# Optimization experiments

Measured on AMD Instinct MI355X. Metric: run time of the kernel, lower is better.

## Reference

```python
import jax, jax.numpy as jnp
import numpy as np

# ---- constants (match init_kwargs) ----
H = 16            # bit depth of location codes
TP = 8            # number of parallel location dims
N = 1 << H        # location magnitude bound
N_K = 2
N_C = 2 * H * N_K + 1   # 65 candidate locations per token
T = 512           # T_train
N_TTNBR = 64
K_VOCAB = 128
S = N_TTNBR + K_VOCAB   # 192
D = 256           # dim_eu
TEMP = 0.05


def cos_similarity(c1, c2):
    """CritiGraph frexp-based cosine: sign product * (1 - bitlength(|a|^|b| + 1)/h)."""
    sg = (2 * (c1 >= 0).astype(jnp.int32) - 1) * (2 * (c2 >= 0).astype(jnp.int32) - 1)
    x = jnp.abs(c1) ^ jnp.abs(c2)
    _, e = jnp.frexp((x + 1).astype(jnp.float32))  # exponent == bit_length(x+1)
    return sg.astype(jnp.float32) * (1.0 - e.astype(jnp.float32) / H)


def setup_inputs() -> dict:
    key = jax.random.key(0)
    ks = jax.random.split(key, 8)
    loc = lambda k, shape: jax.random.randint(k, shape, 1 - N, N, dtype=jnp.int32)
    return {
        "cur_tar": jax.random.randint(ks[0], (T,), 0, K_VOCAB, dtype=jnp.int32),
        "cnc_loc": loc(ks[1], (T, N_C, TP)),
        "sta_loc": loc(ks[2], (T, TP)),
        "ttn_loc": loc(ks[3], (T, N_TTNBR, TP)),
        "voc_loc": loc(ks[4], (T, K_VOCAB, TP)),
        "sta_emb": 0.1 * jax.random.normal(ks[5], (T, D), dtype=jnp.float32),
        "ttn_emb": 0.1 * jax.random.normal(ks[6], (T, N_TTNBR, D), dtype=jnp.float32),
        "voc_emb": 0.1 * jax.random.normal(ks[7], (T, K_VOCAB, D), dtype=jnp.float32),
    }


def reference(cur_tar, cnc_loc, sta_loc, ttn_loc, voc_loc, sta_emb, ttn_emb, voc_emb):
    # positives = dynamic neighbors ++ sampled vocab
    pos_loc = jnp.concatenate([ttn_loc, voc_loc], axis=1)      # (T, S, TP) int32
    pos_emb = jnp.concatenate([ttn_emb, voc_emb], axis=1)      # (T, S, D)

    # Euclidean-space logits
    eu_val = 20.0 * TEMP * jnp.einsum('td,tsd->ts', sta_emb, pos_emb)  # (T, S)

    # CT-space similarities
    cos_sp = cos_similarity(sta_loc[:, None, :], pos_loc)      # (T, S, TP)
    cos_sum = cos_sp.sum(axis=-1)                              # (T, S)
    # candidate location swapped into each track d (ct_val_triton math)
    cos_cp = cos_similarity(cnc_loc[:, None, :, :], pos_loc[:, :, None, :])  # (T, S, N_C, TP)
    ct_val = (cos_sum[:, :, None, None] - cos_sp[:, :, None, :] + cos_cp) / TP \
             * (20.0 * TEMP)                                   # (T, S, N_C, TP)

    # KL(eu || ct) over the dynamic neighbors
    logits_ct_dyn = ct_val[:, :N_TTNBR]                        # (T, Nn, N_C, TP)
    logits_eu_dyn = eu_val[:, :N_TTNBR]                        # (T, Nn)
    p_eu = jax.nn.softmax(logits_eu_dyn, axis=1)
    lp_eu = jax.nn.log_softmax(logits_eu_dyn, axis=1)
    lp_ct = jax.nn.log_softmax(logits_ct_dyn, axis=1)
    loss_dyn_dyn = (p_eu[:, :, None, None] * (lp_eu[:, :, None, None] - lp_ct)).sum(axis=1)  # (T, N_C, TP)

    # cross-entropy over the sampled vocab
    logits_ct_sta = ct_val[:, N_TTNBR:] / TEMP                 # (T, K, N_C, TP)
    logits_flat = logits_ct_sta.reshape(T, K_VOCAB, N_C * TP)
    log_probs = jax.nn.log_softmax(logits_flat, axis=1)        # (T, K, N_C*TP)
    idx = jnp.broadcast_to(cur_tar[:, None, None].astype(jnp.int32), (T, 1, N_C * TP))
    target_lp = jnp.take_along_axis(log_probs, idx, axis=1)[:, 0, :]  # (T, N_C*TP)
    loss_dyn_sta = -target_lp.reshape(T, N_C, TP)              # (T, N_C, TP)

    return loss_dyn_dyn, loss_dyn_sta
```

## Files before the change

kernel.cpp:

```cpp
#include <hip/hip_runtime.h>


#define Tn   512
#define NC   65
#define TPd  8
#define NTn  64
#define KV   128
#define Sn   192
#define Dn   256

__global__ __launch_bounds__(256) void critigraph_kernel(
    const int*   __restrict__ cur_tar,
    const int*   __restrict__ cnc_loc,
    const int*   __restrict__ sta_loc,
    const int*   __restrict__ ttn_loc,
    const int*   __restrict__ voc_loc,
    const float* __restrict__ sta_emb,
    const float* __restrict__ ttn_emb,
    float*       __restrict__ out)
{
    __shared__ int   s_apos[Sn * TPd];
    __shared__ float s_base[Sn * TPd];
    __shared__ float s_csum[Sn];
    __shared__ float s_peu[NTn];
    __shared__ float s_eu[NTn];
    __shared__ int   s_cnc[NC * TPd];
    __shared__ int   s_sta[TPd];
    __shared__ float s_kl;

    const int t    = blockIdx.x;
    const int tid  = threadIdx.x;
    const int lane = tid & 63;
    const int wv   = tid >> 6;

    if (tid < TPd) {
        int v = sta_loc[t * TPd + tid];
        s_sta[tid] = (v < 0) ? (int)(0x80000000u | (unsigned)(-v)) : v;
    }
    for (int i = tid; i < NC * TPd; i += 256) {
        int v = cnc_loc[t * NC * TPd + i];
        s_cnc[i] = (v < 0) ? (int)(0x80000000u | (unsigned)(-v)) : v;
    }
    __syncthreads();

    for (int i = tid; i < Sn * TPd; i += 256) {
        int s = i >> 3;
        int v = (s < NTn) ? ttn_loc[t * NTn * TPd + i]
                          : voc_loc[t * KV * TPd + (i - NTn * TPd)];
        int packed = (v < 0) ? (int)(0x80000000u | (unsigned)(-v)) : v;
        s_apos[i] = packed;
        int   y    = packed ^ s_sta[i & 7];
        int   x    = (y & 0x7fffffff) + 1;
        float fclz = (float)__clz(x);
        float c    = fmaf(fclz, 0.0625f, -1.0f);
        c = __int_as_float(__float_as_int(c) ^ (y & 0x80000000));
        s_base[i] = c;
    }
    __syncthreads();

    if (tid < Sn) {
        float a = 0.f;
        #pragma unroll
        for (int p = 0; p < TPd; ++p) a += s_base[tid * TPd + p];
        s_csum[tid] = a;
    }
    __syncthreads();

    for (int i = tid; i < Sn * TPd; i += 256) {
        int s = i >> 3;
        float scale = (s < NTn) ? 0.125f : 2.5f;
        s_base[i] = (s_csum[s] - s_base[i]) * scale;
    }

    {
        const float4* a4 = (const float4*)(sta_emb + (size_t)t * Dn);
        float4 a = a4[lane];
        for (int s = wv; s < NTn; s += 4) {
            const float4* b4 = (const float4*)(ttn_emb + ((size_t)t * NTn + s) * Dn);
            float4 b = b4[lane];
            float d = a.x * b.x + a.y * b.y + a.z * b.z + a.w * b.w;
            #pragma unroll
            for (int m = 1; m < 64; m <<= 1) d += __shfl_xor(d, m);
            if (lane == 0) s_eu[s] = d;
        }
    }
    __syncthreads();

    if (tid < 64) {
        float e  = s_eu[tid];
        float mx = e;
        #pragma unroll
        for (int m = 1; m < 64; m <<= 1) mx = fmaxf(mx, __shfl_xor(mx, m));
        float ex = __expf(e - mx);
        float z  = ex;
        #pragma unroll
        for (int m = 1; m < 64; m <<= 1) z += __shfl_xor(z, m);
        float pe = ex / z;
        s_peu[tid] = pe;
        float kls = pe * ((e - mx) - __logf(z));
        #pragma unroll
        for (int m = 1; m < 64; m <<= 1) kls += __shfl_xor(kls, m);
        if (tid == 0) s_kl = kls;
    }
    __syncthreads();

    const int   tar = cur_tar[t];
    const float kl  = s_kl;
    const int   g   = lane >> 3;
    const int   sub = lane & 7;
    float* out_dd = out + (size_t)t * NC * TPd;
    float* out_ds = out + (size_t)Tn * NC * TPd + (size_t)t * NC * TPd;

    for (int r = wv; r < NC; r += 4) {
        const int acnc = s_cnc[r * TPd + g];

        float sum = 0.f, dot = 0.f;
        #pragma unroll
        for (int k = 0; k < 8; ++k) {
            int   s    = sub + 8 * k;
            int   y    = s_apos[s * TPd + g] ^ acnc;
            int   x    = (y & 0x7fffffff) + 1;
            float fclz = (float)__clz(x);
            float cc   = fmaf(fclz, 0.0078125f, -0.125f);
            cc = __int_as_float(__float_as_int(cc) ^ (y & 0x80000000));
            float ct = s_base[s * TPd + g] + cc;
            sum += __expf(ct);
            dot  = fmaf(s_peu[s], ct, dot);
        }
        #pragma unroll
        for (int m = 1; m < 8; m <<= 1) {
            sum += __shfl_xor(sum, m);
            dot += __shfl_xor(dot, m);
        }
        float loss_dd = kl - dot + __logf(sum);

        float sum2 = 0.f, tgt = 0.f;
        #pragma unroll
        for (int k = 0; k < 16; ++k) {
            int   vv   = sub + 8 * k;
            int   s    = NTn + vv;
            int   y    = s_apos[s * TPd + g] ^ acnc;
            int   x    = (y & 0x7fffffff) + 1;
            float fclz = (float)__clz(x);
            float cc   = fmaf(fclz, 0.15625f, -2.5f);
            cc = __int_as_float(__float_as_int(cc) ^ (y & 0x80000000));
            float ct20 = s_base[s * TPd + g] + cc;
            sum2 += __expf(ct20);
            tgt = (vv == tar) ? ct20 : tgt;
        }
        #pragma unroll
        for (int m = 1; m < 8; m <<= 1) {
            sum2 += __shfl_xor(sum2, m);
            tgt  += __shfl_xor(tgt, m);
        }
        if (sub == 0) {
            out_dd[r * TPd + g] = loss_dd;
            out_ds[r * TPd + g] = __logf(sum2) - tgt;
        }
    }
}

extern "C" void kernel_launch(void* const* d_in, const int* in_sizes, int n_in,
                              void* d_out, int out_size, void* d_ws, size_t ws_size,
                              hipStream_t stream) {
    (void)in_sizes; (void)n_in; (void)d_ws; (void)ws_size; (void)out_size;
    const int*   cur_tar = (const int*)  d_in[0];
    const int*   cnc_loc = (const int*)  d_in[1];
    const int*   sta_loc = (const int*)  d_in[2];
    const int*   ttn_loc = (const int*)  d_in[3];
    const int*   voc_loc = (const int*)  d_in[4];
    const float* sta_emb = (const float*)d_in[5];
    const float* ttn_emb = (const float*)d_in[6];
    critigraph_kernel<<<Tn, 256, 0, stream>>>(cur_tar, cnc_loc, sta_loc, ttn_loc,
                                              voc_loc, sta_emb, ttn_emb, (float*)d_out);
}
```

Measured before the change: 155.8 us.

## Split candidate rows across two blocks per token and hoist invariant work to registers

Launches two blocks per token, each handling about half of the 65 candidate rows, which doubles grid parallelism but makes both blocks redo the per-token setup (location packing, base cosines, embedding dot, softmax). Folds log2e into the constants so it can use hardware exp2/log2. Interleaves loc and base into an int2 shared array and caches each lane's positives in registers across rows. Replaces the per-row dot and target selection with a precomputed per-track dot base plus a single target lookup. It also adds a launch-bounds occupancy hint, which raises register pressure because of the register-cached arrays.

Result: no change. 155.9 us (+0.0%).

```diff
diff --git a/kernel.cpp b/kernel.cpp
--- a/kernel.cpp
+++ b/kernel.cpp
@@ -9,7 +9,22 @@
 #define Sn   192
 #define Dn   256
 
-__global__ __launch_bounds__(256) void critigraph_kernel(
+#define LOG2E 1.44269504088896340736f
+#define LN2   0.69314718055994530942f
+#define K1D (0.0625f * 0.125f * LOG2E)
+#define K0D (-0.125f * LOG2E)
+#define K1S (0.0625f * 2.5f * LOG2E)
+#define K0S (-2.5f * LOG2E)
+
+__device__ __forceinline__ float exp2_fast(float x) {
+#if __has_builtin(__builtin_amdgcn_exp2f)
+    return __builtin_amdgcn_exp2f(x);
+#else
+    return exp2f(x);
+#endif
+}
+
+__global__ __launch_bounds__(256, 4) void critigraph_kernel(
     const int*   __restrict__ cur_tar,
     const int*   __restrict__ cnc_loc,
     const int*   __restrict__ sta_loc,
@@ -19,16 +34,21 @@
     const float* __restrict__ ttn_emb,
     float*       __restrict__ out)
 {
-    __shared__ int   s_apos[Sn * TPd];
-    __shared__ float s_base[Sn * TPd];
+    __shared__ int2  s_ab[Sn * TPd];
     __shared__ float s_csum[Sn];
     __shared__ float s_peu[NTn];
     __shared__ float s_eu[NTn];
     __shared__ int   s_cnc[NC * TPd];
     __shared__ int   s_sta[TPd];
+    __shared__ float s_dotbase[TPd];
     __shared__ float s_kl;
 
-    const int t    = blockIdx.x;
+    const int bx   = blockIdx.x;
+    const int t    = bx >> 1;
+    const int half = bx & 1;
+    const int c0   = half ? 33 : 0;
+    const int c1   = half ? NC : 33;
+
     const int tid  = threadIdx.x;
     const int lane = tid & 63;
     const int wv   = tid >> 6;
@@ -48,30 +68,13 @@
         int v = (s < NTn) ? ttn_loc[t * NTn * TPd + i]
                           : voc_loc[t * KV * TPd + (i - NTn * TPd)];
         int packed = (v < 0) ? (int)(0x80000000u | (unsigned)(-v)) : v;
-        s_apos[i] = packed;
         int   y    = packed ^ s_sta[i & 7];
         int   x    = (y & 0x7fffffff) + 1;
         float fclz = (float)__clz(x);
         float c    = fmaf(fclz, 0.0625f, -1.0f);
         c = __int_as_float(__float_as_int(c) ^ (y & 0x80000000));
-        s_base[i] = c;
-    }
-    __syncthreads();
-
-    if (tid < Sn) {
-        float a = 0.f;
-        #pragma unroll
-        for (int p = 0; p < TPd; ++p) a += s_base[tid * TPd + p];
-        s_csum[tid] = a;
-    }
-    __syncthreads();
-
-    for (int i = tid; i < Sn * TPd; i += 256) {
-        int s = i >> 3;
-        float scale = (s < NTn) ? 0.125f : 2.5f;
-        s_base[i] = (s_csum[s] - s_base[i]) * scale;
-    }
-
+        s_ab[i] = make_int2(packed, __float_as_int(c));
+    }
     {
         const float4* a4 = (const float4*)(sta_emb + (size_t)t * Dn);
         float4 a = a4[lane];
@@ -86,6 +89,20 @@
     }
     __syncthreads();
 
+    if (tid < Sn) {
+        float a = 0.f;
+        #pragma unroll
+        for (int p = 0; p < TPd; ++p) a += __int_as_float(s_ab[tid * TPd + p].y);
+        s_csum[tid] = a;
+    }
+    __syncthreads();
+
+    for (int i = tid; i < Sn * TPd; i += 256) {
+        int s = i >> 3;
+        float sc = (s < NTn) ? (0.125f * LOG2E) : (2.5f * LOG2E);
+        float sp = __int_as_float(s_ab[i].y);
+        s_ab[i].y = __float_as_int((s_csum[s] - sp) * sc);
+    }
     if (tid < 64) {
         float e  = s_eu[tid];
         float mx = e;
@@ -104,58 +121,85 @@
     }
     __syncthreads();
 
-    const int   tar = cur_tar[t];
-    const float kl  = s_kl;
-    const int   g   = lane >> 3;
-    const int   sub = lane & 7;
+    if (tid < 64) {
+        int g = tid & 7, j = tid >> 3;
+        float a = 0.f;
+        #pragma unroll
+        for (int k = 0; k < 8; ++k) {
+            int s = j * 8 + k;
+            a = fmaf(s_peu[s], __int_as_float(s_ab[s * TPd + g].y), a);
+        }
+        #pragma unroll
+        for (int m = 8; m < 64; m <<= 1) a += __shfl_xor(a, m);
+        if (tid < TPd) s_dotbase[g] = a;
+    }
+    __syncthreads();
+
+    const int g   = lane >> 3;
+    const int sub = lane & 7;
+    const int tar = cur_tar[t];
+
+    float rpeu[8];
+    int2  rdyn[8];
+    int2  rsta[16];
+    #pragma unroll
+    for (int k = 0; k < 8; ++k) {
+        rpeu[k] = s_peu[sub + 8 * k];
+        rdyn[k] = s_ab[(sub + 8 * k) * TPd + g];
+    }
+    #pragma unroll
+    for (int k = 0; k < 16; ++k) rsta[k] = s_ab[(NTn + sub + 8 * k) * TPd + g];
+    const int2  rtar = s_ab[(NTn + tar) * TPd + g];
+    const float dotb = s_dotbase[g];
+    const float kl   = s_kl;
+
     float* out_dd = out + (size_t)t * NC * TPd;
     float* out_ds = out + (size_t)Tn * NC * TPd + (size_t)t * NC * TPd;
 
-    for (int r = wv; r < NC; r += 4) {
+    for (int r = c0 + wv; r < c1; r += 4) {
         const int acnc = s_cnc[r * TPd + g];
 
-        float sum = 0.f, dot = 0.f;
+        float sum = 0.f, dotcc = 0.f;
         #pragma unroll
         for (int k = 0; k < 8; ++k) {
-            int   s    = sub + 8 * k;
-            int   y    = s_apos[s * TPd + g] ^ acnc;
+            int   y    = rdyn[k].x ^ acnc;
             int   x    = (y & 0x7fffffff) + 1;
             float fclz = (float)__clz(x);
-            float cc   = fmaf(fclz, 0.0078125f, -0.125f);
+            float cc   = fmaf(fclz, K1D, K0D);
             cc = __int_as_float(__float_as_int(cc) ^ (y & 0x80000000));
-            float ct = s_base[s * TPd + g] + cc;
-            sum += __expf(ct);
-            dot  = fmaf(s_peu[s], ct, dot);
-        }
-        #pragma unroll
-        for (int m = 1; m < 8; m <<= 1) {
-            sum += __shfl_xor(sum, m);
-            dot += __shfl_xor(dot, m);
-        }
-        float loss_dd = kl - dot + __logf(sum);
-
-        float sum2 = 0.f, tgt = 0.f;
+            sum += exp2_fast(__int_as_float(rdyn[k].y) + cc);
+            dotcc = fmaf(rpeu[k], cc, dotcc);
+        }
+
+        float sum2a = 0.f, sum2b = 0.f;
         #pragma unroll
         for (int k = 0; k < 16; ++k) {
-            int   vv   = sub + 8 * k;
-            int   s    = NTn + vv;
-            int   y    = s_apos[s * TPd + g] ^ acnc;
+            int   y    = rsta[k].x ^ acnc;
             int   x    = (y & 0x7fffffff) + 1;
             float fclz = (float)__clz(x);
-            float cc   = fmaf(fclz, 0.15625f, -2.5f);
+            float cc   = fmaf(fclz, K1S, K0S);
             cc = __int_as_float(__float_as_int(cc) ^ (y & 0x80000000));
-            float ct20 = s_base[s * TPd + g] + cc;
-            sum2 += __expf(ct20);
-            tgt = (vv == tar) ? ct20 : tgt;
-        }
+            float e = exp2_fast(__int_as_float(rsta[k].y) + cc);
+            if (k & 1) sum2b += e; else sum2a += e;
+        }
+        float sum2 = sum2a + sum2b;
+
         #pragma unroll
         for (int m = 1; m < 8; m <<= 1) {
-            sum2 += __shfl_xor(sum2, m);
-            tgt  += __shfl_xor(tgt, m);
-        }
+            sum   += __shfl_xor(sum, m);
+            dotcc += __shfl_xor(dotcc, m);
+            sum2  += __shfl_xor(sum2, m);
+        }
+
         if (sub == 0) {
-            out_dd[r * TPd + g] = loss_dd;
-            out_ds[r * TPd + g] = __logf(sum2) - tgt;
+            int   y    = rtar.x ^ acnc;
+            int   x    = (y & 0x7fffffff) + 1;
+            float fclz = (float)__clz(x);
+            float cc   = fmaf(fclz, K1S, K0S);
+            cc = __int_as_float(__float_as_int(cc) ^ (y & 0x80000000));
+            float tgt2 = __int_as_float(rtar.y) + cc;
+            out_dd[r * TPd + g] = kl + LN2 * (__log2f(sum) - (dotb + dotcc));
+            out_ds[r * TPd + g] = LN2 * (__log2f(sum2) - tgt2);
         }
     }
 }
@@ -171,6 +215,6 @@
     const int*   voc_loc = (const int*)  d_in[4];
     const float* sta_emb = (const float*)d_in[5];
     const float* ttn_emb = (const float*)d_in[6];
-    critigraph_kernel<<<Tn, 256, 0, stream>>>(cur_tar, cnc_loc, sta_loc, ttn_loc,
-                                              voc_loc, sta_emb, ttn_emb, (float*)d_out);
+    critigraph_kernel<<<Tn * 2, 256, 0, stream>>>(cur_tar, cnc_loc, sta_loc, ttn_loc,
+                                                  voc_loc, sta_emb, ttn_emb, (float*)d_out);
 }
```
